# Performance work log

Measured on AMD Instinct MI355X. Metric: run time of the kernel, lower is better.

The kernel has to match this reference:

```python
import jax, jax.numpy as jnp
import numpy as np

EPS_BN = 1e-5
EPS_ATTN = 1e-9


def bn(h, g, b, m, v):
    # inference-mode BatchNorm1d over channel (last) dim
    return (h - m) * (g * jax.lax.rsqrt(v + EPS_BN)) + b


def setup_inputs() -> dict:
    key = jax.random.key(0)
    ks = jax.random.split(key, 16)
    B, N, Cin, C = 16, 2048, 64, 256
    std = 0.05
    inp = {
        "x": jax.random.normal(ks[0], (B, N, Cin), jnp.float32),
        "w1": jax.random.normal(ks[1], (C, Cin), jnp.float32) * std,
        "w2": jax.random.normal(ks[2], (C, C), jnp.float32) * std,
        "wqk": jax.random.normal(ks[3], (C, C), jnp.float32) * std,
        "wv": jax.random.normal(ks[4], (C, C), jnp.float32) * std,
        "bv": jax.random.normal(ks[5], (C,), jnp.float32) * std,
        "wt": jax.random.normal(ks[6], (C, C), jnp.float32) * std,
        "bt": jax.random.normal(ks[7], (C,), jnp.float32) * std,
    }
    for i, name in enumerate(["bn1", "bn2", "bn3"]):
        k = jax.random.split(ks[8 + i], 4)
        inp[name + "_g"] = 1.0 + 0.1 * jax.random.normal(k[0], (C,), jnp.float32)
        inp[name + "_b"] = 0.1 * jax.random.normal(k[1], (C,), jnp.float32)
        inp[name + "_m"] = 0.1 * jax.random.normal(k[2], (C,), jnp.float32)
        inp[name + "_v"] = jax.random.uniform(k[3], (C,), jnp.float32, 0.5, 1.5)
    return inp


def reference(x, w1, w2, wqk, wv, bv, wt, bt,
              bn1_g, bn1_b, bn1_m, bn1_v,
              bn2_g, bn2_b, bn2_m, bn2_v,
              bn3_g, bn3_b, bn3_m, bn3_v):
    # x: [B, N, Cin]; all feature maps kept channel-last [B, N, C]
    h = jax.nn.relu(bn(jnp.einsum('bnc,dc->bnd', x, w1), bn1_g, bn1_b, bn1_m, bn1_v))
    h = jax.nn.relu(bn(jnp.einsum('bnc,dc->bnd', h, w2), bn2_g, bn2_b, bn2_m, bn2_v))

    # SA_Layer: q and k share the same (bias-free) 1x1 conv weights
    q = jnp.einsum('bnc,dc->bnd', h, wqk)          # [B,N,C]
    energy = jnp.einsum('bic,bjc->bij', q, q)      # [B,N,N]
    attn = jax.nn.softmax(energy, axis=-1)
    attn = attn / (EPS_ATTN + jnp.sum(attn, axis=1, keepdims=True))  # L1 renorm over queries
    v = jnp.einsum('bnc,dc->bnd', h, wv) + bv      # [B,N,C]
    x_r = jnp.einsum('bic,bij->bjc', v, attn)      # [B,N,C]

    t = jnp.einsum('bnc,dc->bnd', h - x_r, wt) + bt
    t = jax.nn.relu(bn(t, bn3_g, bn3_b, bn3_m, bn3_v))
    out = h + t                                    # [B,N,C]
    return jnp.transpose(out, (0, 2, 1))           # [B,C,N] as in torch module
```

## Files before the change

kernel.cpp:

```cpp
#include <hip/hip_runtime.h>
#include <hip/hip_bf16.h>

#define B_  16
#define N_  2048
#define C_  256
#define BN_ (B_*N_)

typedef __bf16 bf16x8 __attribute__((ext_vector_type(8)));
typedef float  f32x4  __attribute__((ext_vector_type(4)));
typedef int    i32x4  __attribute__((ext_vector_type(4)));

static __device__ __forceinline__ f32x4 MFMA(bf16x8 a, bf16x8 b, f32x4 c){
  return __builtin_amdgcn_mfma_f32_16x16x32_bf16(a, b, c, 0, 0, 0);
}
static __device__ __forceinline__ unsigned short f2b(float f){
  unsigned int u = __float_as_uint(f);
  u += 0x7fffu + ((u >> 16) & 1u);
  return (unsigned short)(u >> 16);
}

__global__ void prep_kernel(
    const float* __restrict__ w1, const float* __restrict__ w2,
    const float* __restrict__ wqk, const float* __restrict__ wv,
    const float* __restrict__ bv, const float* __restrict__ wt,
    const float* __restrict__ bt,
    const float* __restrict__ g1, const float* __restrict__ b1,
    const float* __restrict__ m1, const float* __restrict__ v1,
    const float* __restrict__ g2, const float* __restrict__ b2,
    const float* __restrict__ m2, const float* __restrict__ v2,
    const float* __restrict__ g3, const float* __restrict__ b3,
    const float* __restrict__ m3, const float* __restrict__ v3,
    unsigned short* __restrict__ w1b, unsigned short* __restrict__ w2b,
    unsigned short* __restrict__ wqkb, unsigned short* __restrict__ wvb,
    unsigned short* __restrict__ wtb,
    float* __restrict__ bias1, float* __restrict__ bias2,
    float* __restrict__ biasv, float* __restrict__ biast)
{
  const int d = blockIdx.x;
  const int c = threadIdx.x;
  const float s1 = g1[d] * rsqrtf(v1[d] + 1e-5f);
  const float s2 = g2[d] * rsqrtf(v2[d] + 1e-5f);
  const float s3 = g3[d] * rsqrtf(v3[d] + 1e-5f);
  if (c < 64) w1b[d*64 + c] = f2b(w1[d*64 + c] * s1);
  w2b[d*256 + c]  = f2b(w2[d*256 + c] * s2);
  wqkb[d*256 + c] = f2b(wqk[d*256 + c]);
  wvb[d*256 + c]  = f2b(wv[d*256 + c]);
  wtb[d*256 + c]  = f2b(wt[d*256 + c] * s3);
  if (c == 0){
    bias1[d] = b1[d] - m1[d]*s1;
    bias2[d] = b2[d] - m2[d]*s2;
    biasv[d] = bv[d];
    biast[d] = bt[d]*s3 + b3[d] - m3[d]*s3;
  }
}

template<int MODE, int K>
__global__ __launch_bounds__(256, 2) void wgemm(
    const void* __restrict__ inp, const unsigned short* __restrict__ wB,
    const float* __restrict__ bias, const float* __restrict__ hf32,
    void* __restrict__ out0, void* __restrict__ out1)
{
  extern __shared__ char smem[];
  unsigned short* Al = (unsigned short*)smem;
  unsigned short* Bl = (unsigned short*)(smem + 64*72*2);
  const int tid  = threadIdx.x;
  const int lane = tid & 63;
  const int w    = tid >> 6;
  const int wr   = w >> 1, wc = w & 1;
  const long row0 = (long)blockIdx.x * 64;

  f32x4 acc[2][8];
  #pragma unroll
  for (int m = 0; m < 2; ++m)
    #pragma unroll
    for (int n = 0; n < 8; ++n) acc[m][n] = f32x4{0.f,0.f,0.f,0.f};

  const int KS = K / 64;
  #pragma unroll 1
  for (int s = 0; s < KS; ++s){
    if (s) __syncthreads();
    if constexpr (MODE == 0){
      const float* xin = (const float*)inp;
      #pragma unroll
      for (int t = 0; t < 4; ++t){
        int idx = tid + t*256;
        int r = idx >> 4, c4 = (idx & 15) * 4;
        float4 v = *(const float4*)(xin + (row0 + r)*K + c4);
        unsigned short* dst = &Al[r*72 + c4];
        dst[0]=f2b(v.x); dst[1]=f2b(v.y); dst[2]=f2b(v.z); dst[3]=f2b(v.w);
      }
    } else {
      const unsigned short* bin = (const unsigned short*)inp;
      #pragma unroll
      for (int t = 0; t < 2; ++t){
        int idx = tid + t*256;
        int r = idx >> 3, c8 = (idx & 7) * 8;
        *(i32x4*)&Al[r*72 + c8] = *(const i32x4*)(bin + (row0 + r)*K + s*64 + c8);
      }
    }
    #pragma unroll
    for (int t = 0; t < 8; ++t){
      int idx = tid + t*256;
      int d = idx >> 3, c8 = (idx & 7) * 8;
      *(i32x4*)&Bl[d*72 + c8] = *(const i32x4*)(wB + d*K + s*64 + c8);
    }
    __syncthreads();
    #pragma unroll
    for (int kk = 0; kk < 2; ++kk){
      bf16x8 a[2], b[8];
      #pragma unroll
      for (int m = 0; m < 2; ++m)
        a[m] = *(const bf16x8*)&Al[(32*wr + 16*m + (lane&15))*72 + kk*32 + (lane>>4)*8];
      #pragma unroll
      for (int n = 0; n < 8; ++n)
        b[n] = *(const bf16x8*)&Bl[(128*wc + 16*n + (lane&15))*72 + kk*32 + (lane>>4)*8];
      #pragma unroll
      for (int m = 0; m < 2; ++m)
        #pragma unroll
        for (int n = 0; n < 8; ++n)
          acc[m][n] = MFMA(a[m], b[n], acc[m][n]);
    }
  }

  if constexpr (MODE <= 2){
    unsigned short* obf = (unsigned short*)out0;
    float* of = (float*)out1;
    #pragma unroll
    for (int n = 0; n < 8; ++n){
      int col = 128*wc + 16*n + (lane&15);
      float bs = 0.f;
      if constexpr (MODE != 2) bs = bias[col];
      #pragma unroll
      for (int m = 0; m < 2; ++m){
        int rl = 32*wr + 16*m + (lane>>4)*4;
        #pragma unroll
        for (int r = 0; r < 4; ++r){
          float v = acc[m][n][r] + bs;
          if constexpr (MODE == 0 || MODE == 1) v = fmaxf(v, 0.f);
          obf[(row0 + rl + r)*256 + col] = f2b(v);
          if constexpr (MODE == 1) of[(row0 + rl + r)*256 + col] = v;
        }
      }
    }
  } else if constexpr (MODE == 3){
    __syncthreads();
    unsigned short* Vl = (unsigned short*)smem;
    #pragma unroll
    for (int n = 0; n < 8; ++n){
      int col = 128*wc + 16*n + (lane&15);
      float bs = bias[col];
      #pragma unroll
      for (int m = 0; m < 2; ++m){
        int rl = 32*wr + 16*m + (lane>>4)*4;
        #pragma unroll
        for (int r = 0; r < 4; ++r)
          Vl[(rl + r)*264 + col] = f2b(acc[m][n][r] + bs);
      }
    }
    __syncthreads();
    long b = row0 >> 11;
    int  n0 = (int)(row0 & 2047);
    unsigned short* vt = (unsigned short*)out0 + b*(256L*2048);
    #pragma unroll 1
    for (int cc = 0; cc < 64; ++cc){
      int c = 64*w + cc;
      vt[(long)c*2048 + n0 + lane] = Vl[lane*264 + c];
    }
  } else {
    __syncthreads();
    float* Ol = (float*)smem;
    #pragma unroll
    for (int n = 0; n < 8; ++n){
      int col = 128*wc + 16*n + (lane&15);
      float bs = bias[col];
      #pragma unroll
      for (int m = 0; m < 2; ++m){
        int rl = 32*wr + 16*m + (lane>>4)*4;
        #pragma unroll
        for (int r = 0; r < 4; ++r){
          float t = fmaxf(acc[m][n][r] + bs, 0.f);
          float h = hf32[(row0 + rl + r)*256 + col];
          Ol[(rl + r)*265 + col] = h + t;
        }
      }
    }
    __syncthreads();
    long b = row0 >> 11;
    int  n0 = (int)(row0 & 2047);
    float* op = (float*)out0 + b*(256L*2048);
    #pragma unroll 1
    for (int cc = 0; cc < 64; ++cc){
      int c = 64*w + cc;
      op[(long)c*2048 + n0 + lane] = Ol[lane*265 + c];
    }
  }
}

__global__ __launch_bounds__(256, 4) void pass1_kernel(
    const unsigned short* __restrict__ q,
    float* __restrict__ rowm, float* __restrict__ rowl)
{
  __shared__ unsigned short qi[64*264];
  __shared__ float smm[4][64], sml[4][64];
  const int tid = threadIdx.x, lane = tid & 63, w = tid >> 6;
  const int l15 = lane & 15, hi = lane >> 4;
  const int lin = blockIdx.y * 32 + blockIdx.x;
  const int swz = (lin & 7) * 64 + (lin >> 3);
  const int b  = swz >> 5;
  const int i0 = (swz & 31) * 64;
  const unsigned short* qb = q + (long)b*N_*C_;

  #pragma unroll
  for (int t = 0; t < 8; ++t){
    int idx = tid + t*256;
    int r = idx >> 5, c8 = (idx & 31) * 8;
    *(i32x4*)&qi[r*264 + c8] = *(const i32x4*)(qb + (long)(i0 + r)*256 + c8);
  }
  __syncthreads();

  float mloc[4], lloc[4];
  #pragma unroll
  for (int ii = 0; ii < 4; ++ii){ mloc[ii] = -3e38f; lloc[ii] = 0.f; }

  #pragma unroll 1
  for (int js = 0; js < 8; ++js){
    const int j0 = js*256 + 64*w;
    #pragma unroll
    for (int h = 0; h < 2; ++h){
      f32x4 e[2][4];
      #pragma unroll
      for (int jf = 0; jf < 2; ++jf)
        #pragma unroll
        for (int ii = 0; ii < 4; ++ii) e[jf][ii] = f32x4{0.f,0.f,0.f,0.f};

      #pragma unroll
      for (int kk = 0; kk < 8; ++kk){
        bf16x8 aa[4], bb[2];
        #pragma unroll
        for (int ii = 0; ii < 4; ++ii)
          aa[ii] = *(const bf16x8*)&qi[(16*ii + l15)*264 + kk*32 + hi*8];
        #pragma unroll
        for (int jf = 0; jf < 2; ++jf)
          bb[jf] = *(const bf16x8*)(qb + (long)(j0 + 16*(2*h + jf) + l15)*256 + kk*32 + hi*8);
        #pragma unroll
        for (int jf = 0; jf < 2; ++jf)
          #pragma unroll
          for (int ii = 0; ii < 4; ++ii)
            e[jf][ii] = MFMA(bb[jf], aa[ii], e[jf][ii]);
      }

      #pragma unroll
      for (int ii = 0; ii < 4; ++ii){
        float tm = fmaxf(fmaxf(fmaxf(e[0][ii][0], e[0][ii][1]), fmaxf(e[0][ii][2], e[0][ii][3])),
                         fmaxf(fmaxf(e[1][ii][0], e[1][ii][1]), fmaxf(e[1][ii][2], e[1][ii][3])));
        float mn = fmaxf(mloc[ii], tm);
        float p = 0.f;
        #pragma unroll
        for (int jf = 0; jf < 2; ++jf)
          #pragma unroll
          for (int r = 0; r < 4; ++r)
            p += __expf(e[jf][ii][r] - mn);
        lloc[ii] = lloc[ii]*__expf(mloc[ii] - mn) + p;
        mloc[ii] = mn;
      }
    }
  }

  #pragma unroll
  for (int ii = 0; ii < 4; ++ii){
    float m0 = mloc[ii], l0 = lloc[ii];
    float mo = __shfl_xor(m0, 16), lo = __shfl_xor(l0, 16);
    float mn = fmaxf(m0, mo);
    l0 = l0*__expf(m0 - mn) + lo*__expf(mo - mn); m0 = mn;
    mo = __shfl_xor(m0, 32); lo = __shfl_xor(l0, 32);
    mn = fmaxf(m0, mo);
    l0 = l0*__expf(m0 - mn) + lo*__expf(mo - mn); m0 = mn;
    if (lane < 16){
      smm[w][16*ii + l15] = m0;
      sml[w][16*ii + l15] = l0;
    }
  }
  __syncthreads();
  if (tid < 64){
    float m0 = smm[0][tid], m1 = smm[1][tid], m2 = smm[2][tid], m3 = smm[3][tid];
    float M = fmaxf(fmaxf(m0, m1), fmaxf(m2, m3));
    float L = sml[0][tid]*__expf(m0 - M) + sml[1][tid]*__expf(m1 - M)
            + sml[2][tid]*__expf(m2 - M) + sml[3][tid]*__expf(m3 - M);
    rowm[(long)b*N_ + i0 + tid] = M;
    rowl[(long)b*N_ + i0 + tid] = L;
  }
}

__global__ __launch_bounds__(256, 2) void pass2_kernel(
    const unsigned short* __restrict__ q, const unsigned short* __restrict__ vT,
    const float* __restrict__ rowm, const float* __restrict__ rowl,
    const float* __restrict__ hf, unsigned short* __restrict__ dbf)
{
  extern __shared__ char smem[];
  unsigned short* qj = (unsigned short*)smem;
  unsigned short* pl = qj + 64*264;
  float* colsum = (float*)(pl + 64*264);
  const int tid = threadIdx.x, lane = tid & 63, w = tid >> 6;
  const int lin = blockIdx.y * 32 + blockIdx.x;
  const int swz = (lin & 7) * 64 + (lin >> 3);
  const int b  = swz >> 5;
  const int j0 = (swz & 31) * 64;
  const unsigned short* qb = q  + (long)b*N_*C_;
  const unsigned short* vb = vT + (long)b*N_*C_;
  const float* mrow = rowm + (long)b*N_;
  const float* lrow = rowl + (long)b*N_;

  #pragma unroll
  for (int t = 0; t < 8; ++t){
    int idx = tid + t*256;
    int r = idx >> 5, c8 = (idx & 31) * 8;
    *(i32x4*)&qj[r*264 + c8] = *(const i32x4*)(qb + (long)(j0 + r)*256 + c8);
  }
  if (tid < 64) colsum[tid] = 0.f;
  __syncthreads();

  float cs[4][4];
  #pragma unroll
  for (int a = 0; a < 4; ++a)
    #pragma unroll
    for (int r = 0; r < 4; ++r) cs[a][r] = 0.f;
  f32x4 nm[4][4];
  #pragma unroll
  for (int a = 0; a < 4; ++a)
    #pragma unroll
    for (int c = 0; c < 4; ++c) nm[a][c] = f32x4{0.f,0.f,0.f,0.f};

  unsigned int pk[4][4][2];

  #pragma unroll 1
  for (int is = 0; is < 8; ++is){
    const int i0 = is * 256;
    const int iw = i0 + 64*w;

    float mi[4], ri[4];
    #pragma unroll
    for (int f = 0; f < 4; ++f){
      int ig = iw + 16*f + (lane&15);
      mi[f] = mrow[ig];
      ri[f] = __builtin_amdgcn_rcpf(lrow[ig]);
    }

    f32x4 e[4][4];
    #pragma unroll
    for (int a = 0; a < 4; ++a)
      #pragma unroll
      for (int f = 0; f < 4; ++f) e[a][f] = f32x4{0.f,0.f,0.f,0.f};
    #pragma unroll
    for (int kk = 0; kk < 8; ++kk){
      bf16x8 a[4], bb[4];
      #pragma unroll
      for (int jf = 0; jf < 4; ++jf)
        a[jf] = *(const bf16x8*)&qj[(16*jf + (lane&15))*264 + kk*32 + (lane>>4)*8];
      #pragma unroll
      for (int f = 0; f < 4; ++f)
        bb[f] = *(const bf16x8*)(qb + (long)(iw + 16*f + (lane&15))*256 + kk*32 + (lane>>4)*8);
      #pragma unroll
      for (int jf = 0; jf < 4; ++jf)
        #pragma unroll
        for (int f = 0; f < 4; ++f)
          e[jf][f] = MFMA(a[jf], bb[f], e[jf][f]);
    }

    if (is > 0){
      const int ip = i0 - 256;
      #pragma unroll
      for (int kc = 0; kc < 8; ++kc){
        bf16x8 pa[4], vv[4];
        #pragma unroll
        for (int jf = 0; jf < 4; ++jf)
          pa[jf] = *(const bf16x8*)&pl[(16*jf + (lane&15))*264 + kc*32 + (lane>>4)*8];
        #pragma unroll
        for (int cf = 0; cf < 4; ++cf)
          vv[cf] = *(const bf16x8*)(vb + (long)(64*w + 16*cf + (lane&15))*2048 + ip + kc*32 + (lane>>4)*8);
        #pragma unroll
        for (int jf = 0; jf < 4; ++jf)
          #pragma unroll
          for (int cf = 0; cf < 4; ++cf)
            nm[jf][cf] = MFMA(pa[jf], vv[cf], nm[jf][cf]);
      }
    }

    #pragma unroll
    for (int f = 0; f < 4; ++f){
      #pragma unroll
      for (int jf = 0; jf < 4; ++jf){
        #pragma unroll
        for (int rp = 0; rp < 2; ++rp){
          float p0 = __expf(e[jf][f][2*rp]   - mi[f]) * ri[f];
          float p1 = __expf(e[jf][f][2*rp+1] - mi[f]) * ri[f];
          cs[jf][2*rp]   += p0;
          cs[jf][2*rp+1] += p1;
          pk[jf][f][rp] = (unsigned int)f2b(p0) | ((unsigned int)f2b(p1) << 16);
        }
      }
    }

    __syncthreads();
    #pragma unroll
    for (int jf = 0; jf < 4; ++jf)
      #pragma unroll
      for (int f = 0; f < 4; ++f)
        #pragma unroll
        for (int rp = 0; rp < 2; ++rp){
          unsigned int v = pk[jf][f][rp];
          int col = 64*w + 16*f + (lane&15);
          pl[(16*jf + (lane>>4)*4 + 2*rp)*264 + col]     = (unsigned short)v;
          pl[(16*jf + (lane>>4)*4 + 2*rp+1)*264 + col]   = (unsigned short)(v >> 16);
        }
    __syncthreads();
  }

  {
    const int ip = 7 * 256;
    #pragma unroll
    for (int kc = 0; kc < 8; ++kc){
      bf16x8 pa[4], vv[4];
      #pragma unroll
      for (int jf = 0; jf < 4; ++jf)
        pa[jf] = *(const bf16x8*)&pl[(16*jf + (lane&15))*264 + kc*32 + (lane>>4)*8];
      #pragma unroll
      for (int cf = 0; cf < 4; ++cf)
        vv[cf] = *(const bf16x8*)(vb + (long)(64*w + 16*cf + (lane&15))*2048 + ip + kc*32 + (lane>>4)*8);
      #pragma unroll
      for (int jf = 0; jf < 4; ++jf)
        #pragma unroll
        for (int cf = 0; cf < 4; ++cf)
          nm[jf][cf] = MFMA(pa[jf], vv[cf], nm[jf][cf]);
    }
  }

  #pragma unroll
  for (int jf = 0; jf < 4; ++jf)
    #pragma unroll
    for (int r = 0; r < 4; ++r){
      float v = cs[jf][r];
      v += __shfl_xor(v, 1); v += __shfl_xor(v, 2);
      v += __shfl_xor(v, 4); v += __shfl_xor(v, 8);
      if ((lane & 15) == 0) atomicAdd(&colsum[16*jf + (lane>>4)*4 + r], v);
    }
  __syncthreads();

  #pragma unroll
  for (int jf = 0; jf < 4; ++jf)
    #pragma unroll
    for (int r = 0; r < 4; ++r){
      int jl = 16*jf + (lane>>4)*4 + r;
      float rcs = __builtin_amdgcn_rcpf(1e-9f + colsum[jl]);
      long rowg = (long)b*N_ + j0 + jl;
      #pragma unroll
      for (int cf = 0; cf < 4; ++cf){
        int c = 64*w + 16*cf + (lane&15);
        float xr = nm[jf][cf][r] * rcs;
        float d = hf[rowg*256 + c] - xr;
        dbf[rowg*256 + c] = f2b(d);
      }
    }
}

extern "C" void kernel_launch(void* const* d_in, const int* in_sizes, int n_in,
                              void* d_out, int out_size, void* d_ws, size_t ws_size,
                              hipStream_t stream)
{
  const float* x   = (const float*)d_in[0];
  const float* w1  = (const float*)d_in[1];
  const float* w2  = (const float*)d_in[2];
  const float* wqk = (const float*)d_in[3];
  const float* wv  = (const float*)d_in[4];
  const float* bv  = (const float*)d_in[5];
  const float* wt  = (const float*)d_in[6];
  const float* bt  = (const float*)d_in[7];
  const float* g1 = (const float*)d_in[8],  *b1 = (const float*)d_in[9];
  const float* m1 = (const float*)d_in[10], *v1 = (const float*)d_in[11];
  const float* g2 = (const float*)d_in[12], *b2 = (const float*)d_in[13];
  const float* m2 = (const float*)d_in[14], *v2 = (const float*)d_in[15];
  const float* g3 = (const float*)d_in[16], *b3 = (const float*)d_in[17];
  const float* m3 = (const float*)d_in[18], *v3 = (const float*)d_in[19];

  char* ws = (char*)d_ws;
  size_t off = 0;
  auto alloc = [&](size_t bytes)->char*{
    char* p = ws + off; off += (bytes + 255) & ~(size_t)255; return p;
  };
  unsigned short* w1b  = (unsigned short*)alloc(256*64*2);
  unsigned short* w2b  = (unsigned short*)alloc(256*256*2);
  unsigned short* wqkb = (unsigned short*)alloc(256*256*2);
  unsigned short* wvb  = (unsigned short*)alloc(256*256*2);
  unsigned short* wtb  = (unsigned short*)alloc(256*256*2);
  float* bias1 = (float*)alloc(256*4);
  float* bias2 = (float*)alloc(256*4);
  float* biasv = (float*)alloc(256*4);
  float* biast = (float*)alloc(256*4);
  unsigned short* h1_bf = (unsigned short*)alloc((size_t)BN_*C_*2);
  float*          h_f32 = (float*)alloc((size_t)BN_*C_*4);
  unsigned short* h_bf  = (unsigned short*)alloc((size_t)BN_*C_*2);
  unsigned short* q_bf  = (unsigned short*)alloc((size_t)BN_*C_*2);
  unsigned short* vT_bf = (unsigned short*)alloc((size_t)BN_*C_*2);
  float* rowm = (float*)alloc((size_t)BN_*4);
  float* rowl = (float*)alloc((size_t)BN_*4);
  unsigned short* d_bf  = (unsigned short*)alloc((size_t)BN_*C_*2);
  (void)ws_size; (void)in_sizes; (void)n_in; (void)out_size;

  hipFuncSetAttribute((const void*)&pass2_kernel,
                      hipFuncAttributeMaxDynamicSharedMemorySize, 67840);
  hipFuncSetAttribute((const void*)&wgemm<4,256>,
                      hipFuncAttributeMaxDynamicSharedMemorySize, 67840);

  prep_kernel<<<256, 256, 0, stream>>>(w1, w2, wqk, wv, bv, wt, bt,
      g1,b1,m1,v1, g2,b2,m2,v2, g3,b3,m3,v3,
      w1b, w2b, wqkb, wvb, wtb, bias1, bias2, biasv, biast);

  wgemm<0,64><<<512, 256, 46080, stream>>>(x, w1b, bias1, nullptr, h1_bf, nullptr);
  wgemm<1,256><<<512, 256, 46080, stream>>>(h1_bf, w2b, bias2, nullptr, h_bf, h_f32);
  wgemm<2,256><<<512, 256, 46080, stream>>>(h_bf, wqkb, nullptr, nullptr, q_bf, nullptr);
  wgemm<3,256><<<512, 256, 46080, stream>>>(h_bf, wvb, biasv, nullptr, vT_bf, nullptr);

  pass1_kernel<<<dim3(32,16), 256, 0, stream>>>(q_bf, rowm, rowl);
  pass2_kernel<<<dim3(32,16), 256, 67840, stream>>>(q_bf, vT_bf, rowm, rowl, h_f32, d_bf);

  wgemm<4,256><<<512, 256, 67840, stream>>>(d_bf, wtb, biast, h_f32, d_out, nullptr);
}
```

Before: 432.2 us.

## Use query self-norm as softmax shift to drop online max in pass1

The Q projection GEMM epilogue now also computes each row's squared norm ||q_i||^2, reduced through shuffles and shared-memory atomics, and writes it into rowm. pass1 uses that precomputed value as a fixed softmax shift, so it only accumulates a plain sum of exponentials. This removes the running-max tracking, the rescaling exps and the max-merge reductions. The trade-off is that ||q_i||^2 is not guaranteed to be the row maximum, since q_i·q_j can exceed it, which risks exp overflow. The self-norm is also taken from fp32 values while the dot products use bf16 q. pass1 additionally lowers its launch-bounds occupancy hint from 4 to 2 and stops unrolling the k loop, which may reduce load/MFMA interleaving.

```diff
diff --git a/kernel.cpp b/kernel.cpp
--- a/kernel.cpp
+++ b/kernel.cpp
@@ -125,6 +125,11 @@
   if constexpr (MODE <= 2){
     unsigned short* obf = (unsigned short*)out0;
     float* of = (float*)out1;
+    float sq[2][4];
+    #pragma unroll
+    for (int m = 0; m < 2; ++m)
+      #pragma unroll
+      for (int r = 0; r < 4; ++r) sq[m][r] = 0.f;
     #pragma unroll
     for (int n = 0; n < 8; ++n){
       int col = 128*wc + 16*n + (lane&15);
@@ -139,8 +144,33 @@
           if constexpr (MODE == 0 || MODE == 1) v = fmaxf(v, 0.f);
           obf[(row0 + rl + r)*256 + col] = f2b(v);
           if constexpr (MODE == 1) of[(row0 + rl + r)*256 + col] = v;
+          if constexpr (MODE == 2) sq[m][r] += v*v;
         }
       }
+    }
+    if constexpr (MODE == 2){
+      #pragma unroll
+      for (int m = 0; m < 2; ++m)
+        #pragma unroll
+        for (int r = 0; r < 4; ++r){
+          float s = sq[m][r];
+          s += __shfl_xor(s, 1); s += __shfl_xor(s, 2);
+          s += __shfl_xor(s, 4); s += __shfl_xor(s, 8);
+          sq[m][r] = s;
+        }
+      __syncthreads();
+      float* ssq = (float*)smem;
+      if (tid < 64) ssq[tid] = 0.f;
+      __syncthreads();
+      if ((lane & 15) == 0){
+        #pragma unroll
+        for (int m = 0; m < 2; ++m)
+          #pragma unroll
+          for (int r = 0; r < 4; ++r)
+            atomicAdd(&ssq[32*wr + 16*m + (lane>>4)*4 + r], sq[m][r]);
+      }
+      __syncthreads();
+      if (tid < 64) ((float*)out1)[row0 + tid] = ssq[tid];
     }
   } else if constexpr (MODE == 3){
     __syncthreads();
@@ -196,12 +226,12 @@
   }
 }
 
-__global__ __launch_bounds__(256, 4) void pass1_kernel(
+__global__ __launch_bounds__(256, 2) void pass1_kernel(
     const unsigned short* __restrict__ q,
-    float* __restrict__ rowm, float* __restrict__ rowl)
+    const float* __restrict__ rowm, float* __restrict__ rowl)
 {
   __shared__ unsigned short qi[64*264];
-  __shared__ float smm[4][64], sml[4][64];
+  __shared__ float sll[4][64];
   const int tid = threadIdx.x, lane = tid & 63, w = tid >> 6;
   const int l15 = lane & 15, hi = lane >> 4;
   const int lin = blockIdx.y * 32 + blockIdx.x;
@@ -216,11 +246,14 @@
     int r = idx >> 5, c8 = (idx & 31) * 8;
     *(i32x4*)&qi[r*264 + c8] = *(const i32x4*)(qb + (long)(i0 + r)*256 + c8);
   }
+
+  float mi[4], lacc[4];
+  #pragma unroll
+  for (int ii = 0; ii < 4; ++ii){
+    mi[ii] = rowm[(long)b*N_ + i0 + 16*ii + l15];
+    lacc[ii] = 0.f;
+  }
   __syncthreads();
-
-  float mloc[4], lloc[4];
-  #pragma unroll
-  for (int ii = 0; ii < 4; ++ii){ mloc[ii] = -3e38f; lloc[ii] = 0.f; }
 
   #pragma unroll 1
   for (int js = 0; js < 8; ++js){
@@ -233,7 +266,7 @@
         #pragma unroll
         for (int ii = 0; ii < 4; ++ii) e[jf][ii] = f32x4{0.f,0.f,0.f,0.f};
 
-      #pragma unroll
+      #pragma unroll 1
       for (int kk = 0; kk < 8; ++kk){
         bf16x8 aa[4], bb[2];
         #pragma unroll
@@ -251,44 +284,27 @@
 
       #pragma unroll
       for (int ii = 0; ii < 4; ++ii){
-        float tm = fmaxf(fmaxf(fmaxf(e[0][ii][0], e[0][ii][1]), fmaxf(e[0][ii][2], e[0][ii][3])),
-                         fmaxf(fmaxf(e[1][ii][0], e[1][ii][1]), fmaxf(e[1][ii][2], e[1][ii][3])));
-        float mn = fmaxf(mloc[ii], tm);
         float p = 0.f;
         #pragma unroll
         for (int jf = 0; jf < 2; ++jf)
           #pragma unroll
           for (int r = 0; r < 4; ++r)
-            p += __expf(e[jf][ii][r] - mn);
-        lloc[ii] = lloc[ii]*__expf(mloc[ii] - mn) + p;
-        mloc[ii] = mn;
+            p += __expf(e[jf][ii][r] - mi[ii]);
+        lacc[ii] += p;
       }
     }
   }
 
   #pragma unroll
   for (int ii = 0; ii < 4; ++ii){
-    float m0 = mloc[ii], l0 = lloc[ii];
-    float mo = __shfl_xor(m0, 16), lo = __shfl_xor(l0, 16);
-    float mn = fmaxf(m0, mo);
-    l0 = l0*__expf(m0 - mn) + lo*__expf(mo - mn); m0 = mn;
-    mo = __shfl_xor(m0, 32); lo = __shfl_xor(l0, 32);
-    mn = fmaxf(m0, mo);
-    l0 = l0*__expf(m0 - mn) + lo*__expf(mo - mn); m0 = mn;
-    if (lane < 16){
-      smm[w][16*ii + l15] = m0;
-      sml[w][16*ii + l15] = l0;
-    }
+    float l0 = lacc[ii];
+    l0 += __shfl_xor(l0, 16);
+    l0 += __shfl_xor(l0, 32);
+    if (lane < 16) sll[w][16*ii + l15] = l0;
   }
   __syncthreads();
-  if (tid < 64){
-    float m0 = smm[0][tid], m1 = smm[1][tid], m2 = smm[2][tid], m3 = smm[3][tid];
-    float M = fmaxf(fmaxf(m0, m1), fmaxf(m2, m3));
-    float L = sml[0][tid]*__expf(m0 - M) + sml[1][tid]*__expf(m1 - M)
-            + sml[2][tid]*__expf(m2 - M) + sml[3][tid]*__expf(m3 - M);
-    rowm[(long)b*N_ + i0 + tid] = M;
-    rowl[(long)b*N_ + i0 + tid] = L;
-  }
+  if (tid < 64)
+    rowl[(long)b*N_ + i0 + tid] = sll[0][tid] + sll[1][tid] + sll[2][tid] + sll[3][tid];
 }
 
 __global__ __launch_bounds__(256, 2) void pass2_kernel(
@@ -516,7 +532,7 @@
 
   wgemm<0,64><<<512, 256, 46080, stream>>>(x, w1b, bias1, nullptr, h1_bf, nullptr);
   wgemm<1,256><<<512, 256, 46080, stream>>>(h1_bf, w2b, bias2, nullptr, h_bf, h_f32);
-  wgemm<2,256><<<512, 256, 46080, stream>>>(h_bf, wqkb, nullptr, nullptr, q_bf, nullptr);
+  wgemm<2,256><<<512, 256, 46080, stream>>>(h_bf, wqkb, nullptr, nullptr, q_bf, rowm);
   wgemm<3,256><<<512, 256, 46080, stream>>>(h_bf, wvb, biasv, nullptr, vT_bf, nullptr);
 
   pass1_kernel<<<dim3(32,16), 256, 0, stream>>>(q_bf, rowm, rowl);
```

After: 360.7 us. 16.6% less time.
